# Performance work log

Hardware: AMD Instinct MI355X
Metric: run time of the kernel (lower is better)

Reference implementation:

```python
import jax, jax.numpy as jnp
import numpy as np
import math

INPUT_SIZE = 2048
OUTPUT_SIZE = 10000
EPS = 1e-8


def _hadamard_cropped(rows, cols):
    # Sylvester Hadamard: H[i, j] = (-1) ** popcount(i & j), built only on the
    i = np.arange(rows, dtype=np.int64)[:, None]
    j = np.arange(cols, dtype=np.int64)[None, :]
    a = i & j
    nbits = max(rows, cols).bit_length()
    parity = np.zeros((rows, cols), dtype=np.int64)
    for k in range(nbits):
        parity += (a >> k) & 1
    return (1 - 2 * (parity & 1)).astype(np.float32)


def setup_inputs() -> dict:
    key = jax.random.key(0)
    kx, kb = jax.random.split(key)
    init_scale = 1.0 / math.sqrt(OUTPUT_SIZE)
    x = jax.random.normal(kx, (16384, INPUT_SIZE), dtype=jnp.float32)
    proj = jnp.asarray(_hadamard_cropped(OUTPUT_SIZE, INPUT_SIZE))
    scale = jnp.full((1,), init_scale, dtype=jnp.float32)
    bias = jax.random.uniform(kb, (OUTPUT_SIZE,), dtype=jnp.float32,
                              minval=-init_scale, maxval=init_scale)
    return {"x": x, "proj": proj, "scale": scale, "bias": bias}


def reference(x, proj, scale, bias):
    # L2-normalize along last dim (norm + eps, matching torch semantics)
    xn = x / (jnp.linalg.norm(x, axis=-1, keepdims=True) + EPS)
    # linear with cropped Hadamard matrix: [B, in] @ [out, in]^T -> [B, out]
    out = -scale * jnp.einsum('bi,oi->bo', xn, proj)
    return out + bias[None, :]
```

## Files before the change

### kernel.cpp

```cpp
#include <hip/hip_runtime.h>
#include <math.h>


typedef float f32x4 __attribute__((ext_vector_type(4)));

constexpr int N_IN  = 2048;
constexpr int N_OUT = 10000;
constexpr int ROWS_PER_BLOCK = 4;

__global__ __launch_bounds__(256, 4) void fwht_proj_kernel(
    const float* __restrict__ x,
    const float* __restrict__ scale,
    const float* __restrict__ bias,
    float* __restrict__ out)
{
    __shared__ f32x4 biaslds[N_OUT / 4];

    {
        const f32x4* __restrict__ b4 = reinterpret_cast<const f32x4*>(bias);
        for (int i = threadIdx.x; i < N_OUT / 4; i += 256)
            biaslds[i] = b4[i];
    }
    __syncthreads();

    const int wave = threadIdx.x >> 6;
    const int lane = threadIdx.x & 63;
    const int row  = (blockIdx.x << 2) + wave;

    const float* __restrict__ xrow = x + (size_t)row * N_IN;

    f32x4 v[8];
    float ss = 0.0f;
#pragma unroll
    for (int j = 0; j < 8; ++j) {
        v[j] = *reinterpret_cast<const f32x4*>(xrow + (j << 8) + (lane << 2));
        ss = fmaf(v[j].x, v[j].x, ss);
        ss = fmaf(v[j].y, v[j].y, ss);
        ss = fmaf(v[j].z, v[j].z, ss);
        ss = fmaf(v[j].w, v[j].w, ss);
    }
#pragma unroll
    for (int m = 1; m < 64; m <<= 1)
        ss += __shfl_xor(ss, m, 64);
    const float inv = 1.0f / (sqrtf(ss) + 1e-8f);

#pragma unroll
    for (int j = 0; j < 8; ++j) {
        const f32x4 a = v[j];
        f32x4 t;
        t.x = a.x + a.y;  t.y = a.x - a.y;
        t.z = a.z + a.w;  t.w = a.z - a.w;
        f32x4 u;
        u.x = t.x + t.z;  u.y = t.y + t.w;
        u.z = t.x - t.z;  u.w = t.y - t.w;
        v[j] = u;
    }
#pragma unroll
    for (int m = 1; m <= 32; m <<= 1) {
        const bool lo = (lane & m) == 0;
#pragma unroll
        for (int j = 0; j < 8; ++j) {
            f32x4 o;
            o.x = __shfl_xor(v[j].x, m, 64);
            o.y = __shfl_xor(v[j].y, m, 64);
            o.z = __shfl_xor(v[j].z, m, 64);
            o.w = __shfl_xor(v[j].w, m, 64);
            v[j] = lo ? (v[j] + o) : (o - v[j]);
        }
    }
#pragma unroll
    for (int jm = 1; jm <= 4; jm <<= 1) {
#pragma unroll
        for (int j = 0; j < 8; ++j) {
            if ((j & jm) == 0) {
                const f32x4 a = v[j], b = v[j ^ jm];
                v[j]      = a + b;
                v[j ^ jm] = a - b;
            }
        }
    }

    const float s = -scale[0] * inv;
    float* __restrict__ orow = out + (size_t)row * N_OUT;

#pragma unroll
    for (int w = 0; w < 4; ++w) {
#pragma unroll 4
        for (int j = 0; j < 8; ++j) {
            const int o = (w << 11) + (j << 8) + (lane << 2);
            const f32x4 b = biaslds[(w << 9) + (j << 6) + lane];
            f32x4 r;
            r.x = fmaf(s, v[j].x, b.x);
            r.y = fmaf(s, v[j].y, b.y);
            r.z = fmaf(s, v[j].z, b.z);
            r.w = fmaf(s, v[j].w, b.w);
            *reinterpret_cast<f32x4*>(orow + o) = r;
        }
    }
#pragma unroll 4
    for (int j = 0; j < 7; ++j) {
        const int o = 8192 + (j << 8) + (lane << 2);
        const f32x4 b = biaslds[2048 + (j << 6) + lane];
        f32x4 r;
        r.x = fmaf(s, v[j].x, b.x);
        r.y = fmaf(s, v[j].y, b.y);
        r.z = fmaf(s, v[j].z, b.z);
        r.w = fmaf(s, v[j].w, b.w);
        *reinterpret_cast<f32x4*>(orow + o) = r;
    }
    if (lane < 4) {
        const int o = 9984 + (lane << 2);
        const f32x4 b = biaslds[2496 + lane];
        f32x4 r;
        r.x = fmaf(s, v[7].x, b.x);
        r.y = fmaf(s, v[7].y, b.y);
        r.z = fmaf(s, v[7].z, b.z);
        r.w = fmaf(s, v[7].w, b.w);
        *reinterpret_cast<f32x4*>(orow + o) = r;
    }
}

extern "C" void kernel_launch(void* const* d_in, const int* in_sizes, int n_in,
                              void* d_out, int out_size, void* d_ws, size_t ws_size,
                              hipStream_t stream) {
    const float* x     = (const float*)d_in[0];
    const float* scale = (const float*)d_in[2];
    const float* bias  = (const float*)d_in[3];
    float* out = (float*)d_out;

    const int rows = in_sizes[0] / N_IN;
    dim3 grid(rows / ROWS_PER_BLOCK), block(256);
    hipLaunchKernelGGL(fwht_proj_kernel, grid, block, 0, stream,
                       x, scale, bias, out);
}
```

Measured before the change: 164.7 us.

## Process four rows per wave with register prefetch of the next row

Each wave now handles four consecutive rows instead of one, loading the next row's input into registers while the current row is normalized, transformed and written. This amortizes the per-block bias copy into LDS over more rows and overlaps global loads with the shuffle-based Hadamard transform and output stores. In exchange it doubles register use for the row buffers, which may lower occupancy, and launches a grid four times smaller.

```diff
diff --git a/kernel.cpp b/kernel.cpp
--- a/kernel.cpp
+++ b/kernel.cpp
@@ -6,7 +6,8 @@
 
 constexpr int N_IN  = 2048;
 constexpr int N_OUT = 10000;
-constexpr int ROWS_PER_BLOCK = 4;
+constexpr int WAVES_PER_BLOCK = 4;
+constexpr int ROWS_PER_WAVE   = 4;
 
 __global__ __launch_bounds__(256, 4) void fwht_proj_kernel(
     const float* __restrict__ x,
@@ -25,98 +26,118 @@
 
     const int wave = threadIdx.x >> 6;
     const int lane = threadIdx.x & 63;
-    const int row  = (blockIdx.x << 2) + wave;
+    const size_t wrow0 = ((size_t)blockIdx.x * WAVES_PER_BLOCK + wave) * ROWS_PER_WAVE;
+    const float sc = scale[0];
 
-    const float* __restrict__ xrow = x + (size_t)row * N_IN;
-
-    f32x4 v[8];
-    float ss = 0.0f;
+    f32x4 cur[8], nxt[8];
+    {
+        const float* __restrict__ xr = x + wrow0 * N_IN;
 #pragma unroll
-    for (int j = 0; j < 8; ++j) {
-        v[j] = *reinterpret_cast<const f32x4*>(xrow + (j << 8) + (lane << 2));
-        ss = fmaf(v[j].x, v[j].x, ss);
-        ss = fmaf(v[j].y, v[j].y, ss);
-        ss = fmaf(v[j].z, v[j].z, ss);
-        ss = fmaf(v[j].w, v[j].w, ss);
+        for (int j = 0; j < 8; ++j)
+            cur[j] = *reinterpret_cast<const f32x4*>(xr + (j << 8) + (lane << 2));
     }
-#pragma unroll
-    for (int m = 1; m < 64; m <<= 1)
-        ss += __shfl_xor(ss, m, 64);
-    const float inv = 1.0f / (sqrtf(ss) + 1e-8f);
 
 #pragma unroll
-    for (int j = 0; j < 8; ++j) {
-        const f32x4 a = v[j];
-        f32x4 t;
-        t.x = a.x + a.y;  t.y = a.x - a.y;
-        t.z = a.z + a.w;  t.w = a.z - a.w;
-        f32x4 u;
-        u.x = t.x + t.z;  u.y = t.y + t.w;
-        u.z = t.x - t.z;  u.w = t.y - t.w;
-        v[j] = u;
-    }
+    for (int r = 0; r < ROWS_PER_WAVE; ++r) {
+        if (r + 1 < ROWS_PER_WAVE) {
+            const float* __restrict__ xr = x + (wrow0 + r + 1) * N_IN;
 #pragma unroll
-    for (int m = 1; m <= 32; m <<= 1) {
-        const bool lo = (lane & m) == 0;
+            for (int j = 0; j < 8; ++j)
+                nxt[j] = *reinterpret_cast<const f32x4*>(xr + (j << 8) + (lane << 2));
+        }
+
+        float ss = 0.0f;
 #pragma unroll
         for (int j = 0; j < 8; ++j) {
-            f32x4 o;
-            o.x = __shfl_xor(v[j].x, m, 64);
-            o.y = __shfl_xor(v[j].y, m, 64);
-            o.z = __shfl_xor(v[j].z, m, 64);
-            o.w = __shfl_xor(v[j].w, m, 64);
-            v[j] = lo ? (v[j] + o) : (o - v[j]);
+            ss = fmaf(cur[j].x, cur[j].x, ss);
+            ss = fmaf(cur[j].y, cur[j].y, ss);
+            ss = fmaf(cur[j].z, cur[j].z, ss);
+            ss = fmaf(cur[j].w, cur[j].w, ss);
         }
-    }
 #pragma unroll
-    for (int jm = 1; jm <= 4; jm <<= 1) {
+        for (int m = 1; m < 64; m <<= 1)
+            ss += __shfl_xor(ss, m, 64);
+        const float inv = 1.0f / (sqrtf(ss) + 1e-8f);
+
 #pragma unroll
         for (int j = 0; j < 8; ++j) {
-            if ((j & jm) == 0) {
-                const f32x4 a = v[j], b = v[j ^ jm];
-                v[j]      = a + b;
-                v[j ^ jm] = a - b;
+            const f32x4 a = cur[j];
+            f32x4 t;
+            t.x = a.x + a.y;  t.y = a.x - a.y;
+            t.z = a.z + a.w;  t.w = a.z - a.w;
+            f32x4 u;
+            u.x = t.x + t.z;  u.y = t.y + t.w;
+            u.z = t.x - t.z;  u.w = t.y - t.w;
+            cur[j] = u;
+        }
+#pragma unroll
+        for (int m = 1; m <= 32; m <<= 1) {
+            const bool lo = (lane & m) == 0;
+#pragma unroll
+            for (int j = 0; j < 8; ++j) {
+                f32x4 o;
+                o.x = __shfl_xor(cur[j].x, m, 64);
+                o.y = __shfl_xor(cur[j].y, m, 64);
+                o.z = __shfl_xor(cur[j].z, m, 64);
+                o.w = __shfl_xor(cur[j].w, m, 64);
+                cur[j] = lo ? (cur[j] + o) : (o - cur[j]);
             }
         }
-    }
+#pragma unroll
+        for (int jm = 1; jm <= 4; jm <<= 1) {
+#pragma unroll
+            for (int j = 0; j < 8; ++j) {
+                if ((j & jm) == 0) {
+                    const f32x4 a = cur[j], b = cur[j ^ jm];
+                    cur[j]      = a + b;
+                    cur[j ^ jm] = a - b;
+                }
+            }
+        }
 
-    const float s = -scale[0] * inv;
-    float* __restrict__ orow = out + (size_t)row * N_OUT;
+        const float s = -sc * inv;
+        float* __restrict__ orow = out + (wrow0 + r) * N_OUT;
+#pragma unroll
+        for (int w = 0; w < 4; ++w) {
+#pragma unroll 4
+            for (int j = 0; j < 8; ++j) {
+                const int o = (w << 11) + (j << 8) + (lane << 2);
+                const f32x4 b = biaslds[(w << 9) + (j << 6) + lane];
+                f32x4 rv;
+                rv.x = fmaf(s, cur[j].x, b.x);
+                rv.y = fmaf(s, cur[j].y, b.y);
+                rv.z = fmaf(s, cur[j].z, b.z);
+                rv.w = fmaf(s, cur[j].w, b.w);
+                *reinterpret_cast<f32x4*>(orow + o) = rv;
+            }
+        }
+#pragma unroll 4
+        for (int j = 0; j < 7; ++j) {
+            const int o = 8192 + (j << 8) + (lane << 2);
+            const f32x4 b = biaslds[2048 + (j << 6) + lane];
+            f32x4 rv;
+            rv.x = fmaf(s, cur[j].x, b.x);
+            rv.y = fmaf(s, cur[j].y, b.y);
+            rv.z = fmaf(s, cur[j].z, b.z);
+            rv.w = fmaf(s, cur[j].w, b.w);
+            *reinterpret_cast<f32x4*>(orow + o) = rv;
+        }
+        if (lane < 4) {
+            const int o = 9984 + (lane << 2);
+            const f32x4 b = biaslds[2496 + lane];
+            f32x4 rv;
+            rv.x = fmaf(s, cur[7].x, b.x);
+            rv.y = fmaf(s, cur[7].y, b.y);
+            rv.z = fmaf(s, cur[7].z, b.z);
+            rv.w = fmaf(s, cur[7].w, b.w);
+            *reinterpret_cast<f32x4*>(orow + o) = rv;
+        }
 
+        if (r + 1 < ROWS_PER_WAVE) {
 #pragma unroll
-    for (int w = 0; w < 4; ++w) {
-#pragma unroll 4
-        for (int j = 0; j < 8; ++j) {
-            const int o = (w << 11) + (j << 8) + (lane << 2);
-            const f32x4 b = biaslds[(w << 9) + (j << 6) + lane];
-            f32x4 r;
-            r.x = fmaf(s, v[j].x, b.x);
-            r.y = fmaf(s, v[j].y, b.y);
-            r.z = fmaf(s, v[j].z, b.z);
-            r.w = fmaf(s, v[j].w, b.w);
-            *reinterpret_cast<f32x4*>(orow + o) = r;
+            for (int j = 0; j < 8; ++j)
+                cur[j] = nxt[j];
         }
-    }
-#pragma unroll 4
-    for (int j = 0; j < 7; ++j) {
-        const int o = 8192 + (j << 8) + (lane << 2);
-        const f32x4 b = biaslds[2048 + (j << 6) + lane];
-        f32x4 r;
-        r.x = fmaf(s, v[j].x, b.x);
-        r.y = fmaf(s, v[j].y, b.y);
-        r.z = fmaf(s, v[j].z, b.z);
-        r.w = fmaf(s, v[j].w, b.w);
-        *reinterpret_cast<f32x4*>(orow + o) = r;
-    }
-    if (lane < 4) {
-        const int o = 9984 + (lane << 2);
-        const f32x4 b = biaslds[2496 + lane];
-        f32x4 r;
-        r.x = fmaf(s, v[7].x, b.x);
-        r.y = fmaf(s, v[7].y, b.y);
-        r.z = fmaf(s, v[7].z, b.z);
-        r.w = fmaf(s, v[7].w, b.w);
-        *reinterpret_cast<f32x4*>(orow + o) = r;
     }
 }
 
@@ -129,7 +150,7 @@
     float* out = (float*)d_out;
 
     const int rows = in_sizes[0] / N_IN;
-    dim3 grid(rows / ROWS_PER_BLOCK), block(256);
+    dim3 grid(rows / (WAVES_PER_BLOCK * ROWS_PER_WAVE)), block(256);
     hipLaunchKernelGGL(fwht_proj_kernel, grid, block, 0, stream,
                        x, scale, bias, out);
 }
```

Result: slower. 169.3 us (+2.8%).
